# Kernel tuning notes

Measured on AMD Instinct MI355X. Metric: run time of the kernel, lower is better.

## Reference

```python
import jax, jax.numpy as jnp
import numpy as np

N_USER = 50000
N_ITEM = 100000
D = 64            # embed_size; layer_size = [64, 64, 64]
NL = 3            # number of propagation layers
NNZ = 2400000     # nonzeros of sparse Laplacian L
B = 1024          # batch of (user, pos_item, neg_item)
N = N_USER + N_ITEM


def setup_inputs() -> dict:
    key = jax.random.key(0)
    ks = jax.random.split(key, 20)
    inp = {}
    # learned parameters
    inp["user_emb"] = jax.random.normal(ks[0], (N_USER, D), jnp.float32) * 0.1
    inp["item_emb"] = jax.random.normal(ks[1], (N_ITEM, D), jnp.float32) * 0.1
    inp["lin1_w"] = jax.random.normal(ks[2], (4, D // 2), jnp.float32) * 0.5
    inp["lin1_b"] = jnp.zeros((D // 2,), jnp.float32)
    inp["lin2_w"] = jax.random.normal(ks[3], (D // 2, D), jnp.float32) * 0.2
    inp["lin2_b"] = jnp.zeros((D,), jnp.float32)
    inp["w1"] = jax.random.normal(ks[4], (NL, D, D), jnp.float32) * (1.0 / np.sqrt(D))
    inp["b1"] = jnp.zeros((NL, D), jnp.float32)
    inp["w2"] = jax.random.normal(ks[5], (NL, D, D), jnp.float32) * (1.0 / np.sqrt(D))
    inp["b2"] = jnp.zeros((NL, D), jnp.float32)
    # sparse normalized Laplacian L in COO form (eye_mat handled as +E)
    inp["lap_row"] = jax.random.randint(ks[6], (NNZ,), 0, N, jnp.int32)
    inp["lap_col"] = jax.random.randint(ks[7], (NNZ,), 0, N, jnp.int32)
    inp["lap_val"] = jax.random.uniform(ks[8], (NNZ,), jnp.float32) * (1.0 / 16.0)
    # forward args
    inp["user_idx"] = jax.random.randint(ks[9], (B,), 0, N_USER, jnp.int32)
    inp["user_feat"] = jax.random.normal(ks[10], (B, 4), jnp.float32)
    inp["pos_idx"] = jax.random.randint(ks[11], (B,), 0, N_ITEM, jnp.int32)
    inp["neg_idx"] = jax.random.randint(ks[12], (B,), 0, N_ITEM, jnp.int32)
    inp["mlp_ratio"] = jnp.float32(0.5)
    return inp


def reference(user_emb, item_emb, user_feat, lin1_w, lin1_b, lin2_w, lin2_b,
              w1, b1, w2, b2, lap_val, mlp_ratio,
              lap_row, lap_col, user_idx, pos_idx, neg_idx):
    n_user = user_emb.shape[0]
    n_nodes = user_emb.shape[0] + item_emb.shape[0]

    # user MLP: two stacked Linears (no activation in between, per Sequential)
    user_mlp = (user_feat @ lin1_w + lin1_b) @ lin2_w + lin2_b  # [B, D]
    # in-place no_grad embedding blend (stop_gradient mirrors torch.no_grad on mlp path)
    upd = user_emb[user_idx] * (1.0 - mlp_ratio) + jax.lax.stop_gradient(user_mlp) * mlp_ratio
    ue = user_emb.at[user_idx].set(upd)

    E = jnp.concatenate([ue, item_emb], axis=0)  # [N, D]

    def spmm(X):
        # L @ X via gather-multiply-segment_sum over COO nonzeros
        return jax.ops.segment_sum(lap_val[:, None] * X[lap_col], lap_row,
                                   num_segments=n_nodes)

    all_E = [E]
    for k in range(w1.shape[0]):
        L_E = spmm(E)                 # L @ E
        L_I_E = L_E + E               # (L + I) @ E
        msg = (L_I_E @ w1[k] + b1[k]) + ((L_E * E) @ w2[k] + b2[k])
        E = jax.nn.leaky_relu(msg, negative_slope=0.2)
        # F.normalize(E, p=2, dim=1) with eps=1e-12
        norm = E / jnp.maximum(jnp.linalg.norm(E, axis=1, keepdims=True), 1e-12)
        all_E.append(norm)

    all_E = jnp.concatenate(all_E, axis=1)  # [N, D*(NL+1)]
    users = all_E[:n_user]
    items = all_E[n_user:]
    return (users[user_idx], items[pos_idx], items[neg_idx])
```

## Files before the change

### kernel.cpp

```cpp
#include <hip/hip_runtime.h>
#include <hip/hip_bf16.h>

#define N_USERC 50000
#define N_ITEMC 100000
#define NNODE   150000
#define DIM     64
#define NLAYERS 3
#define NNZC    2400000
#define BATCH   1024

#define RPB     128
#define NBUCK   1172
#define NCHUNK  512
#define CHUNK   4688
#define CAPB    3072

using short8 = __attribute__((ext_vector_type(8))) short;
using f32x4  = __attribute__((ext_vector_type(4))) float;

__device__ __forceinline__ float bf2f(ushort u) {
    return __uint_as_float(((unsigned)u) << 16);
}
__device__ __forceinline__ ushort f2bf(float f) {
    unsigned u = __float_as_uint(f);
    u += 0x7FFF + ((u >> 16) & 1);
    return (ushort)(u >> 16);
}

__device__ __forceinline__ int block_excl_scan(int v, int* lds) {
    int lane = threadIdx.x & 63;
    int wid  = threadIdx.x >> 6;
    int nw   = (blockDim.x + 63) >> 6;
    int inc = v;
#pragma unroll
    for (int o = 1; o < 64; o <<= 1) {
        int n = __shfl_up(inc, o, 64);
        if (lane >= o) inc += n;
    }
    if (lane == 63) lds[wid] = inc;
    __syncthreads();
    if (wid == 0) {
        int tv = (lane < nw) ? lds[lane] : 0;
#pragma unroll
        for (int o = 1; o < 16; o <<= 1) {
            int n = __shfl_up(tv, o, 64);
            if (lane >= o) tv += n;
        }
        if (lane < nw) lds[lane] = tv;
    }
    __syncthreads();
    int woff = (wid == 0) ? 0 : lds[wid - 1];
    return woff + (inc - v);
}

__global__ void k_copy_E(const float* __restrict__ ue, const float* __restrict__ ie,
                         ushort* __restrict__ Ebf) {
    int i = blockIdx.x * blockDim.x + threadIdx.x;
    const int userEnd = N_USERC * DIM / 4;
    const int total   = NNODE * DIM / 4;
    if (i < total) {
        float4 v;
        if (i < userEnd) v = ((const float4*)ue)[i];
        else             v = ((const float4*)ie)[i - userEnd];
        ushort4 b;
        b.x = f2bf(v.x); b.y = f2bf(v.y); b.z = f2bf(v.z); b.w = f2bf(v.w);
        ((ushort4*)Ebf)[i] = b;
    }
}

__global__ void k_winner(const int* __restrict__ user_idx, int* __restrict__ winner) {
    int b = blockIdx.x * blockDim.x + threadIdx.x;
    if (b < BATCH) atomicMax(&winner[user_idx[b]], b);
}

__global__ void k_mlp_update(const float* __restrict__ user_emb,
                             const float* __restrict__ user_feat,
                             const float* __restrict__ l1w, const float* __restrict__ l1b,
                             const float* __restrict__ l2w, const float* __restrict__ l2b,
                             const float* __restrict__ ratio_p,
                             const int* __restrict__ user_idx,
                             const int* __restrict__ winner,
                             ushort* __restrict__ Ebf) {
    int b = blockIdx.x;
    int d = threadIdx.x;
    int u = user_idx[b];
    if (winner[u] != b) return;
    float ratio = ratio_p[0];
    float uf0 = user_feat[b * 4 + 0], uf1 = user_feat[b * 4 + 1];
    float uf2 = user_feat[b * 4 + 2], uf3 = user_feat[b * 4 + 3];
    float acc = l2b[d];
#pragma unroll
    for (int j = 0; j < 32; ++j) {
        float h = l1b[j] + uf0 * l1w[0 * 32 + j] + uf1 * l1w[1 * 32 + j]
                         + uf2 * l1w[2 * 32 + j] + uf3 * l1w[3 * 32 + j];
        acc += h * l2w[j * DIM + d];
    }
    float v = user_emb[u * DIM + d] * (1.f - ratio) + acc * ratio;
    Ebf[u * DIM + d] = f2bf(v);
}

__global__ void k_prepW(const float* __restrict__ w1, const float* __restrict__ w2,
                        ushort* __restrict__ Wtg) {
    int i = blockIdx.x * blockDim.x + threadIdx.x;
    if (i >= NLAYERS * 64 * 128) return;
    int layer = i >> 13;
    int rem = i & 8191;
    int n = rem >> 7, kk = rem & 127;
    float v = (kk < 64) ? w1[layer * 4096 + kk * 64 + n]
                        : w2[layer * 4096 + (kk - 64) * 64 + n];
    Wtg[i] = f2bf(v);
}

__global__ __launch_bounds__(256) void k_chunksort(const int* __restrict__ rows,
                                                   const int* __restrict__ cols,
                                                   const float* __restrict__ vals,
                                                   unsigned long long* __restrict__ tmp,
                                                   ushort* __restrict__ scanus) {
    __shared__ int hist[NBUCK];
    __shared__ int sutil[16];
    __shared__ unsigned long long stag[CHUNK];

    const int c = blockIdx.x;
    const int s = c * CHUNK;
    const int e = (s + CHUNK < NNZC) ? s + CHUNK : NNZC;
    const int t = threadIdx.x;

    for (int i = t; i < NBUCK; i += 256) hist[i] = 0;
    __syncthreads();
    for (int i = s + t; i < e; i += 256) atomicAdd(&hist[rows[i] >> 7], 1);
    __syncthreads();

    int loc[5];
    int sum = 0;
#pragma unroll
    for (int k = 0; k < 5; ++k) {
        int idx = t * 5 + k;
        int v = (idx < NBUCK) ? hist[idx] : 0;
        loc[k] = sum;
        sum += v;
    }
    int excl = block_excl_scan(sum, sutil);
#pragma unroll
    for (int k = 0; k < 5; ++k) {
        int idx = t * 5 + k;
        if (idx < NBUCK) hist[idx] = excl + loc[k];
    }
    __syncthreads();

    for (int i = t; i < NBUCK; i += 256) scanus[(size_t)c * (NBUCK + 1) + i] = (ushort)hist[i];
    if (t == 0) scanus[(size_t)c * (NBUCK + 1) + NBUCK] = (ushort)(e - s);
    __syncthreads();

    for (int i = s + t; i < e; i += 256) {
        int r = rows[i];
        int b = r >> 7, ro = r & 127;
        unsigned hi = ((unsigned)ro << 18) | (unsigned)cols[i];
        unsigned long long pk = ((unsigned long long)hi << 32) | (unsigned)__float_as_uint(vals[i]);
        int pos = atomicAdd(&hist[b], 1);
        stag[pos] = pk;
    }
    __syncthreads();

    int n = e - s;
    for (int i = t; i < n; i += 256) tmp[s + i] = stag[i];
}

__global__ void k_buckcnt(const ushort* __restrict__ scanus, int* __restrict__ bcnt) {
    int b = blockIdx.x * blockDim.x + threadIdx.x;
    if (b >= NBUCK) return;
    int sum = 0;
    for (int c = 0; c < NCHUNK; ++c) {
        const ushort* row = scanus + (size_t)c * (NBUCK + 1);
        sum += (int)row[b + 1] - (int)row[b];
    }
    bcnt[b] = sum;
}

__global__ __launch_bounds__(256) void k_bscan(const int* __restrict__ bcnt,
                                               int* __restrict__ bstart,
                                               int* __restrict__ rowptr) {
    __shared__ int sutil[16];
    int t = threadIdx.x;
    int loc[5];
    int sum = 0;
#pragma unroll
    for (int k = 0; k < 5; ++k) {
        int idx = t * 5 + k;
        int v = (idx < NBUCK) ? bcnt[idx] : 0;
        loc[k] = sum;
        sum += v;
    }
    int excl = block_excl_scan(sum, sutil);
#pragma unroll
    for (int k = 0; k < 5; ++k) {
        int idx = t * 5 + k;
        if (idx < NBUCK) bstart[idx] = excl + loc[k];
    }
    if (t == 0) { bstart[NBUCK] = NNZC; rowptr[NNODE] = NNZC; }
}

__global__ __launch_bounds__(256) void k_compact(const ushort* __restrict__ scanus,
                                                 const int* __restrict__ bstart,
                                                 const unsigned long long* __restrict__ tmp,
                                                 unsigned long long* __restrict__ csr,
                                                 int* __restrict__ rowptr) {
    __shared__ int runstart[NCHUNK];
    __shared__ int pref[NCHUNK + 1];
    __shared__ int sutil[16];
    __shared__ int rcur[RPB];
    __shared__ unsigned long long stag[CAPB];
    const int b = blockIdx.x;
    const int t = threadIdx.x;

    for (int r = t; r < NCHUNK; r += 256) {
        const ushort* row = scanus + (size_t)r * (NBUCK + 1);
        int s0 = row[b], s1 = row[b + 1];
        runstart[r] = r * CHUNK + s0;
        pref[r] = s1 - s0;
    }
    if (t < RPB) rcur[t] = 0;
    __syncthreads();
    int v0 = pref[t * 2], v1 = pref[t * 2 + 1];
    int sum = v0 + v1;
    int excl = block_excl_scan(sum, sutil);
    pref[t * 2] = excl;
    pref[t * 2 + 1] = excl + v0;
    if (t == 255) pref[NCHUNK] = excl + sum;
    __syncthreads();

    const int total = pref[NCHUNK];
    const int obase = bstart[b];

    if (total <= CAPB) {
        for (int r = t; r < NCHUNK; r += 256) {
            int p0 = pref[r], p1 = pref[r + 1];
            int rs = runstart[r];
            for (int i = p0; i < p1; ++i) stag[i] = tmp[rs + (i - p0)];
        }
        __syncthreads();
        for (int i = t; i < total; i += 256)
            atomicAdd(&rcur[(int)(stag[i] >> 50) & 127], 1);
        __syncthreads();
        int rv = (t < RPB) ? rcur[t] : 0;
        int rex = block_excl_scan(rv, sutil);
        if (t < RPB) {
            rcur[t] = rex;
            int grow = b * RPB + t;
            if (grow < NNODE) rowptr[grow] = obase + rex;
        }
        __syncthreads();
        for (int i = t; i < total; i += 256) {
            unsigned long long pk = stag[i];
            int ro = (int)(pk >> 50) & 127;
            int pos = atomicAdd(&rcur[ro], 1);
            csr[obase + pos] = pk;
        }
        return;
    }

    for (int i = t; i < total; i += 256) {
        int lo = 0, hi = NCHUNK - 1;
        while (lo < hi) {
            int mid = (lo + hi + 1) >> 1;
            if (pref[mid] <= i) lo = mid; else hi = mid - 1;
        }
        unsigned long long pk = tmp[runstart[lo] + (i - pref[lo])];
        atomicAdd(&rcur[(int)(pk >> 50) & 127], 1);
    }
    __syncthreads();
    int rv = (t < RPB) ? rcur[t] : 0;
    int rex = block_excl_scan(rv, sutil);
    if (t < RPB) {
        rcur[t] = rex;
        int grow = b * RPB + t;
        if (grow < NNODE) rowptr[grow] = obase + rex;
    }
    __syncthreads();
    for (int i = t; i < total; i += 256) {
        int lo = 0, hi = NCHUNK - 1;
        while (lo < hi) {
            int mid = (lo + hi + 1) >> 1;
            if (pref[mid] <= i) lo = mid; else hi = mid - 1;
        }
        unsigned long long pk = tmp[runstart[lo] + (i - pref[lo])];
        int ro = (int)(pk >> 50) & 127;
        int pos = atomicAdd(&rcur[ro], 1);
        csr[obase + pos] = pk;
    }
}

__global__ __launch_bounds__(256) void k_spmm(const int* __restrict__ rowptr,
                                              const unsigned long long* __restrict__ csr,
                                              const ushort* __restrict__ Ebf,
                                              float* __restrict__ L) {
    int lane = threadIdx.x & 63;
    int row  = blockIdx.x * 4 + (threadIdx.x >> 6);
    row = __builtin_amdgcn_readfirstlane(row);
    if (row >= NNODE) return;
    int s = __builtin_amdgcn_readfirstlane(rowptr[row]);
    int e = __builtin_amdgcn_readfirstlane(rowptr[row + 1]);
    const ushort* Ep = Ebf + lane;
    float acc = 0.f;
    int j = s;
    for (; j + 16 <= e; j += 16) {
        unsigned long long pk[16];
        float ev[16];
#pragma unroll
        for (int k = 0; k < 16; ++k) pk[k] = csr[j + k];
#pragma unroll
        for (int k = 0; k < 16; ++k) {
            int col = (int)(pk[k] >> 32) & 0x3FFFF;
            ev[k] = bf2f(Ep[col * DIM]);
        }
#pragma unroll
        for (int k = 0; k < 16; ++k)
            acc += __uint_as_float((unsigned)pk[k]) * ev[k];
    }
    if (j < e) {
        int m = e - j;
        unsigned long long pk[16];
        float ev[16];
#pragma unroll
        for (int k = 0; k < 16; ++k) {
            int idx = j + (k < m ? k : m - 1);
            pk[k] = csr[idx];
        }
#pragma unroll
        for (int k = 0; k < 16; ++k) {
            int col = (int)(pk[k] >> 32) & 0x3FFFF;
            ev[k] = bf2f(Ep[col * DIM]);
        }
#pragma unroll
        for (int k = 0; k < 16; ++k) {
            unsigned v = (k < m) ? (unsigned)pk[k] : 0u;
            acc += __uint_as_float(v) * ev[k];
        }
    }
    L[row * DIM + lane] = acc;
}

__global__ __launch_bounds__(256) void k_transform(const float* __restrict__ L,
                                                   const ushort* __restrict__ Ebf_in,
                                                   const ushort* __restrict__ Wtg,
                                                   const float* __restrict__ b1k,
                                                   const float* __restrict__ b2k,
                                                   ushort* __restrict__ Ebf_out) {
    __shared__ ushort A_s[64 * 136];
    __shared__ ushort W_s[64 * 136];
    __shared__ float  bias_s[64];

    const int t = threadIdx.x;
    const int rowbase = blockIdx.x * 64;
    if (t < 64) bias_s[t] = b1k[t] + b2k[t];

#pragma unroll
    for (int it = 0; it < 4; ++it) {
        int task = t + 256 * it;
        int n = task >> 4, k = (task & 15) * 8;
        uint4 wv = *(const uint4*)&Wtg[n * 128 + k];
        *(uint4*)&W_s[n * 136 + k] = wv;
    }
#pragma unroll
    for (int it = 0; it < 4; ++it) {
        int task = t + 256 * it;
        int rl = task >> 4, col = (task & 15) * 4;
        int row = rowbase + rl;
        float4 l4 = make_float4(0.f, 0.f, 0.f, 0.f);
        float e0 = 0.f, e1 = 0.f, e2 = 0.f, e3 = 0.f;
        if (row < NNODE) {
            l4 = *(const float4*)&L[row * 64 + col];
            ushort4 ub = *(const ushort4*)&Ebf_in[row * 64 + col];
            e0 = bf2f(ub.x); e1 = bf2f(ub.y); e2 = bf2f(ub.z); e3 = bf2f(ub.w);
        }
        *(ushort4*)&A_s[rl * 136 + col] =
            make_ushort4(f2bf(l4.x + e0), f2bf(l4.y + e1), f2bf(l4.z + e2), f2bf(l4.w + e3));
        *(ushort4*)&A_s[rl * 136 + 64 + col] =
            make_ushort4(f2bf(l4.x * e0), f2bf(l4.y * e1), f2bf(l4.z * e2), f2bf(l4.w * e3));
    }
    __syncthreads();

    const int w = t >> 6, l = t & 63;
    const int m16 = l & 15;
    const int q   = l >> 4;
    const int lm  = w * 16 + m16;

    f32x4 z = {0.f, 0.f, 0.f, 0.f};
    f32x4 acc[4] = {z, z, z, z};
#pragma unroll
    for (int ks = 0; ks < 4; ++ks) {
        short8 af = *(const short8*)&A_s[lm * 136 + ks * 32 + q * 8];
#pragma unroll
        for (int nt = 0; nt < 4; ++nt) {
            short8 wf = *(const short8*)&W_s[(nt * 16 + m16) * 136 + ks * 32 + q * 8];
            acc[nt] = __builtin_amdgcn_mfma_f32_16x16x32_bf16(af, wf, acc[nt], 0, 0, 0);
        }
    }
    __syncthreads();

    float* Cs = (float*)A_s;
#pragma unroll
    for (int nt = 0; nt < 4; ++nt) {
        int col = nt * 16 + m16;
#pragma unroll
        for (int r = 0; r < 4; ++r) {
            int lrow = w * 16 + q * 4 + r;
            Cs[lrow * 68 + col] = acc[nt][r];
        }
    }
    __syncthreads();

#pragma unroll
    for (int it = 0; it < 2; ++it) {
        int task = t + 256 * it;
        int rl = task >> 3, col = (task & 7) * 8;
        int row = rowbase + rl;
        if (row < NNODE) {
            float4 v0 = *(const float4*)&Cs[rl * 68 + col];
            float4 v1 = *(const float4*)&Cs[rl * 68 + col + 4];
            float o[8] = {v0.x, v0.y, v0.z, v0.w, v1.x, v1.y, v1.z, v1.w};
            ushort ob[8];
#pragma unroll
            for (int j = 0; j < 8; ++j) {
                float v = o[j] + bias_s[col + j];
                v = v >= 0.f ? v : 0.2f * v;
                ob[j] = f2bf(v);
            }
            uint4 pb;
            pb.x = (unsigned)ob[0] | ((unsigned)ob[1] << 16);
            pb.y = (unsigned)ob[2] | ((unsigned)ob[3] << 16);
            pb.z = (unsigned)ob[4] | ((unsigned)ob[5] << 16);
            pb.w = (unsigned)ob[6] | ((unsigned)ob[7] << 16);
            *(uint4*)&Ebf_out[row * 64 + col] = pb;
        }
    }
}

__global__ __launch_bounds__(256) void k_gather(const ushort* __restrict__ Ebf,
                                                const int* __restrict__ user_idx,
                                                const int* __restrict__ pos_idx,
                                                const int* __restrict__ neg_idx,
                                                float* __restrict__ out,
                                                int seg, int normalize) {
    int wid  = threadIdx.x >> 6;
    int lane = threadIdx.x & 63;
    int o = blockIdx.x * 4 + wid;
    if (o >= 3 * BATCH) return;
    int g = o >> 10, b = o & 1023;
    int row;
    if (g == 0)      row = user_idx[b];
    else if (g == 1) row = N_USERC + pos_idx[b];
    else             row = N_USERC + neg_idx[b];
    float v = bf2f(Ebf[row * DIM + lane]);
    if (normalize) {
        float ss = v * v;
#pragma unroll
        for (int m = 32; m; m >>= 1) ss += __shfl_xor(ss, m, 64);
        float nrm = sqrtf(ss);
        nrm = fmaxf(nrm, 1e-12f);
        v = v / nrm;
    }
    out[(g * BATCH + b) * 256 + seg * 64 + lane] = v;
}

extern "C" void kernel_launch(void* const* d_in, const int* in_sizes, int n_in,
                              void* d_out, int out_size, void* d_ws, size_t ws_size,
                              hipStream_t stream) {
    const float* user_emb  = (const float*)d_in[0];
    const float* item_emb  = (const float*)d_in[1];
    const float* lin1_w    = (const float*)d_in[2];
    const float* lin1_b    = (const float*)d_in[3];
    const float* lin2_w    = (const float*)d_in[4];
    const float* lin2_b    = (const float*)d_in[5];
    const float* w1        = (const float*)d_in[6];
    const float* b1        = (const float*)d_in[7];
    const float* w2        = (const float*)d_in[8];
    const float* b2        = (const float*)d_in[9];
    const int*   lap_row   = (const int*)d_in[10];
    const int*   lap_col   = (const int*)d_in[11];
    const float* lap_val   = (const float*)d_in[12];
    const int*   user_idx  = (const int*)d_in[13];
    const float* user_feat = (const float*)d_in[14];
    const int*   pos_idx   = (const int*)d_in[15];
    const int*   neg_idx   = (const int*)d_in[16];
    const float* mlp_ratio = (const float*)d_in[17];
    float* out = (float*)d_out;

    size_t off = 0;
    auto carve = [&](size_t bytes) { size_t r = off; off = (off + bytes + 255) & ~(size_t)255; return r; };
    size_t oL      = carve((size_t)NNODE * DIM * 4);
    size_t oEbf    = carve((size_t)NNODE * DIM * 2);
    size_t oCsr    = carve((size_t)NNZC * 8);
    size_t oScan   = carve((size_t)NCHUNK * (NBUCK + 1) * 2);
    size_t oBcnt   = carve((size_t)NBUCK * 4);
    size_t oBstart = carve((size_t)(NBUCK + 1) * 4);
    size_t oRowptr = carve((size_t)(NNODE + 1) * 4);
    size_t oWinner = carve((size_t)N_USERC * 4);
    (void)ws_size;

    char* base = (char*)d_ws;
    float*              L      = (float*)(base + oL);
    unsigned long long* tmp    = (unsigned long long*)(base + oL);
    ushort*             Ebf    = (ushort*)(base + oEbf);
    unsigned long long* csr    = (unsigned long long*)(base + oCsr);
    ushort*             scanus = (ushort*)(base + oScan);
    int*                bcnt   = (int*)(base + oBcnt);
    int*                bstart = (int*)(base + oBstart);
    int*                rowptr = (int*)(base + oRowptr);
    int*                winner = (int*)(base + oWinner);
    ushort*             Wtg    = (ushort*)(base + oScan);

    k_chunksort<<<NCHUNK, 256, 0, stream>>>(lap_row, lap_col, lap_val, tmp, scanus);
    k_buckcnt<<<(NBUCK + 255) / 256, 256, 0, stream>>>(scanus, bcnt);
    k_bscan<<<1, 256, 0, stream>>>(bcnt, bstart, rowptr);
    k_compact<<<NBUCK, 256, 0, stream>>>(scanus, bstart, tmp, csr, rowptr);

    k_prepW<<<(NLAYERS * 64 * 128 + 255) / 256, 256, 0, stream>>>(w1, w2, Wtg);
    hipMemsetAsync(winner, 0xFF, (size_t)N_USERC * 4, stream);
    k_copy_E<<<(NNODE * DIM / 4 + 255) / 256, 256, 0, stream>>>(user_emb, item_emb, Ebf);
    k_winner<<<(BATCH + 255) / 256, 256, 0, stream>>>(user_idx, winner);
    k_mlp_update<<<BATCH, 64, 0, stream>>>(user_emb, user_feat, lin1_w, lin1_b,
                                           lin2_w, lin2_b, mlp_ratio, user_idx, winner, Ebf);
    k_gather<<<(3 * BATCH) / 4, 256, 0, stream>>>(Ebf, user_idx, pos_idx, neg_idx, out, 0, 0);

    for (int k = 0; k < NLAYERS; ++k) {
        k_spmm<<<(NNODE + 3) / 4, 256, 0, stream>>>(rowptr, csr, Ebf, L);
        k_transform<<<(NNODE + 63) / 64, 256, 0, stream>>>(
            L, Ebf, Wtg + (size_t)k * 64 * 128, b1 + (size_t)k * DIM,
            b2 + (size_t)k * DIM, Ebf);
        k_gather<<<(3 * BATCH) / 4, 256, 0, stream>>>(Ebf, user_idx, pos_idx, neg_idx,
                                                      out, k + 1, 1);
    }
}
```

Before: 464.9 us.

## Fuse (L+I)E and L*E prep into SpMM, persistent grid, parallel bucket count

SpMM now computes both transform inputs, L_E+E and L_E*E, and writes them as bf16 into a 128-wide buffer with nontemporal stores. The transform kernel then just copies that buffer into LDS instead of reading fp32 L plus E. The SpMM becomes a grid-stride persistent kernel with 8/4-wide tail steps instead of a padded 16-wide tail. Bucket counting is split across 8 chunk partitions and summed in the scan kernel, raising parallelism in preprocessing. The bf16 intermediate equals the old rounding in the transform, so accuracy is unchanged, but the SpMM does more per-row work and issues an extra E read.

```diff
diff --git a/kernel.cpp b/kernel.cpp
--- a/kernel.cpp
+++ b/kernel.cpp
@@ -14,9 +14,11 @@
 #define NCHUNK  512
 #define CHUNK   4688
 #define CAPB    3072
+#define NPARTB  8
 
 using short8 = __attribute__((ext_vector_type(8))) short;
 using f32x4  = __attribute__((ext_vector_type(4))) float;
+using uintx4 = __attribute__((ext_vector_type(4))) unsigned;
 
 __device__ __forceinline__ float bf2f(ushort u) {
     return __uint_as_float(((unsigned)u) << 16);
@@ -165,18 +167,21 @@
     for (int i = t; i < n; i += 256) tmp[s + i] = stag[i];
 }
 
-__global__ void k_buckcnt(const ushort* __restrict__ scanus, int* __restrict__ bcnt) {
-    int b = blockIdx.x * blockDim.x + threadIdx.x;
+__global__ __launch_bounds__(256) void k_buckcnt(const ushort* __restrict__ scanus,
+                                                 int* __restrict__ bcntp) {
+    int b = blockIdx.x * 256 + threadIdx.x;
+    int g = blockIdx.y;
     if (b >= NBUCK) return;
+    int c0 = g * (NCHUNK / NPARTB), c1 = c0 + NCHUNK / NPARTB;
     int sum = 0;
-    for (int c = 0; c < NCHUNK; ++c) {
+    for (int c = c0; c < c1; ++c) {
         const ushort* row = scanus + (size_t)c * (NBUCK + 1);
         sum += (int)row[b + 1] - (int)row[b];
     }
-    bcnt[b] = sum;
-}
-
-__global__ __launch_bounds__(256) void k_bscan(const int* __restrict__ bcnt,
+    bcntp[g * NBUCK + b] = sum;
+}
+
+__global__ __launch_bounds__(256) void k_bscan(const int* __restrict__ bcntp,
                                                int* __restrict__ bstart,
                                                int* __restrict__ rowptr) {
     __shared__ int sutil[16];
@@ -186,7 +191,11 @@
 #pragma unroll
     for (int k = 0; k < 5; ++k) {
         int idx = t * 5 + k;
-        int v = (idx < NBUCK) ? bcnt[idx] : 0;
+        int v = 0;
+        if (idx < NBUCK) {
+#pragma unroll
+            for (int g = 0; g < NPARTB; ++g) v += bcntp[g * NBUCK + idx];
+        }
         loc[k] = sum;
         sum += v;
     }
@@ -289,58 +298,65 @@
     }
 }
 
+template<int K>
+__device__ __forceinline__ float gacc_full(const unsigned long long* __restrict__ csr,
+                                           const ushort* __restrict__ Ep, int j) {
+    unsigned long long pk[K];
+    float ev[K];
+#pragma unroll
+    for (int k = 0; k < K; ++k) pk[k] = csr[j + k];
+#pragma unroll
+    for (int k = 0; k < K; ++k) {
+        int col = (int)(pk[k] >> 32) & 0x3FFFF;
+        ev[k] = bf2f(Ep[col * DIM]);
+    }
+    float a = 0.f;
+#pragma unroll
+    for (int k = 0; k < K; ++k)
+        a += __uint_as_float((unsigned)pk[k]) * ev[k];
+    return a;
+}
+
 __global__ __launch_bounds__(256) void k_spmm(const int* __restrict__ rowptr,
                                               const unsigned long long* __restrict__ csr,
                                               const ushort* __restrict__ Ebf,
-                                              float* __restrict__ L) {
-    int lane = threadIdx.x & 63;
-    int row  = blockIdx.x * 4 + (threadIdx.x >> 6);
-    row = __builtin_amdgcn_readfirstlane(row);
-    if (row >= NNODE) return;
-    int s = __builtin_amdgcn_readfirstlane(rowptr[row]);
-    int e = __builtin_amdgcn_readfirstlane(rowptr[row + 1]);
+                                              ushort* __restrict__ Abf) {
+    const int lane = threadIdx.x & 63;
+    const int nw = gridDim.x * 4;
     const ushort* Ep = Ebf + lane;
-    float acc = 0.f;
-    int j = s;
-    for (; j + 16 <= e; j += 16) {
-        unsigned long long pk[16];
-        float ev[16];
-#pragma unroll
-        for (int k = 0; k < 16; ++k) pk[k] = csr[j + k];
-#pragma unroll
-        for (int k = 0; k < 16; ++k) {
-            int col = (int)(pk[k] >> 32) & 0x3FFFF;
-            ev[k] = bf2f(Ep[col * DIM]);
-        }
-#pragma unroll
-        for (int k = 0; k < 16; ++k)
-            acc += __uint_as_float((unsigned)pk[k]) * ev[k];
-    }
-    if (j < e) {
-        int m = e - j;
-        unsigned long long pk[16];
-        float ev[16];
-#pragma unroll
-        for (int k = 0; k < 16; ++k) {
-            int idx = j + (k < m ? k : m - 1);
-            pk[k] = csr[idx];
-        }
-#pragma unroll
-        for (int k = 0; k < 16; ++k) {
-            int col = (int)(pk[k] >> 32) & 0x3FFFF;
-            ev[k] = bf2f(Ep[col * DIM]);
-        }
-#pragma unroll
-        for (int k = 0; k < 16; ++k) {
-            unsigned v = (k < m) ? (unsigned)pk[k] : 0u;
-            acc += __uint_as_float(v) * ev[k];
-        }
-    }
-    L[row * DIM + lane] = acc;
-}
-
-__global__ __launch_bounds__(256) void k_transform(const float* __restrict__ L,
-                                                   const ushort* __restrict__ Ebf_in,
+    for (int row0 = blockIdx.x * 4 + (threadIdx.x >> 6); row0 < NNODE; row0 += nw) {
+        int row = __builtin_amdgcn_readfirstlane(row0);
+        int s = __builtin_amdgcn_readfirstlane(rowptr[row]);
+        int e = __builtin_amdgcn_readfirstlane(rowptr[row + 1]);
+        float acc = 0.f;
+        int j = s;
+        for (; j + 16 <= e; j += 16) acc += gacc_full<16>(csr, Ep, j);
+        if (j + 8 <= e) { acc += gacc_full<8>(csr, Ep, j); j += 8; }
+        if (j + 4 <= e) { acc += gacc_full<4>(csr, Ep, j); j += 4; }
+        if (j < e) {
+            int m = e - j;
+            unsigned long long pk[4];
+            float ev[4];
+#pragma unroll
+            for (int k = 0; k < 4; ++k) pk[k] = csr[j + (k < m ? k : m - 1)];
+#pragma unroll
+            for (int k = 0; k < 4; ++k) {
+                int col = (int)(pk[k] >> 32) & 0x3FFFF;
+                ev[k] = bf2f(Ep[col * DIM]);
+            }
+#pragma unroll
+            for (int k = 0; k < 4; ++k) {
+                unsigned v = (k < m) ? (unsigned)pk[k] : 0u;
+                acc += __uint_as_float(v) * ev[k];
+            }
+        }
+        float eo = bf2f(Ebf[row * DIM + lane]);
+        __builtin_nontemporal_store(f2bf(acc + eo), &Abf[row * 128 + lane]);
+        __builtin_nontemporal_store(f2bf(acc * eo), &Abf[row * 128 + 64 + lane]);
+    }
+}
+
+__global__ __launch_bounds__(256) void k_transform(const ushort* __restrict__ Abf,
                                                    const ushort* __restrict__ Wtg,
                                                    const float* __restrict__ b1k,
                                                    const float* __restrict__ b2k,
@@ -363,19 +379,12 @@
 #pragma unroll
     for (int it = 0; it < 4; ++it) {
         int task = t + 256 * it;
-        int rl = task >> 4, col = (task & 15) * 4;
+        int rl = task >> 4, k8 = (task & 15) * 8;
         int row = rowbase + rl;
-        float4 l4 = make_float4(0.f, 0.f, 0.f, 0.f);
-        float e0 = 0.f, e1 = 0.f, e2 = 0.f, e3 = 0.f;
-        if (row < NNODE) {
-            l4 = *(const float4*)&L[row * 64 + col];
-            ushort4 ub = *(const ushort4*)&Ebf_in[row * 64 + col];
-            e0 = bf2f(ub.x); e1 = bf2f(ub.y); e2 = bf2f(ub.z); e3 = bf2f(ub.w);
-        }
-        *(ushort4*)&A_s[rl * 136 + col] =
-            make_ushort4(f2bf(l4.x + e0), f2bf(l4.y + e1), f2bf(l4.z + e2), f2bf(l4.w + e3));
-        *(ushort4*)&A_s[rl * 136 + 64 + col] =
-            make_ushort4(f2bf(l4.x * e0), f2bf(l4.y * e1), f2bf(l4.z * e2), f2bf(l4.w * e3));
+        uintx4 v = {0u, 0u, 0u, 0u};
+        if (row < NNODE)
+            v = __builtin_nontemporal_load((const uintx4*)&Abf[row * 128 + k8]);
+        *(uintx4*)&A_s[rl * 136 + k8] = v;
     }
     __syncthreads();
 
@@ -495,23 +504,24 @@
     size_t oBstart = carve((size_t)(NBUCK + 1) * 4);
     size_t oRowptr = carve((size_t)(NNODE + 1) * 4);
     size_t oWinner = carve((size_t)N_USERC * 4);
-    (void)ws_size;
+    size_t oBcntP  = carve((size_t)NPARTB * NBUCK * 4);
+    (void)ws_size; (void)oBcnt;
 
     char* base = (char*)d_ws;
-    float*              L      = (float*)(base + oL);
+    ushort*             Abf    = (ushort*)(base + oL);
     unsigned long long* tmp    = (unsigned long long*)(base + oL);
     ushort*             Ebf    = (ushort*)(base + oEbf);
     unsigned long long* csr    = (unsigned long long*)(base + oCsr);
     ushort*             scanus = (ushort*)(base + oScan);
-    int*                bcnt   = (int*)(base + oBcnt);
     int*                bstart = (int*)(base + oBstart);
     int*                rowptr = (int*)(base + oRowptr);
     int*                winner = (int*)(base + oWinner);
+    int*                bcntp  = (int*)(base + oBcntP);
     ushort*             Wtg    = (ushort*)(base + oScan);
 
     k_chunksort<<<NCHUNK, 256, 0, stream>>>(lap_row, lap_col, lap_val, tmp, scanus);
-    k_buckcnt<<<(NBUCK + 255) / 256, 256, 0, stream>>>(scanus, bcnt);
-    k_bscan<<<1, 256, 0, stream>>>(bcnt, bstart, rowptr);
+    k_buckcnt<<<dim3(5, NPARTB), 256, 0, stream>>>(scanus, bcntp);
+    k_bscan<<<1, 256, 0, stream>>>(bcntp, bstart, rowptr);
     k_compact<<<NBUCK, 256, 0, stream>>>(scanus, bstart, tmp, csr, rowptr);
 
     k_prepW<<<(NLAYERS * 64 * 128 + 255) / 256, 256, 0, stream>>>(w1, w2, Wtg);
@@ -523,9 +533,9 @@
     k_gather<<<(3 * BATCH) / 4, 256, 0, stream>>>(Ebf, user_idx, pos_idx, neg_idx, out, 0, 0);
 
     for (int k = 0; k < NLAYERS; ++k) {
-        k_spmm<<<(NNODE + 3) / 4, 256, 0, stream>>>(rowptr, csr, Ebf, L);
+        k_spmm<<<2048, 256, 0, stream>>>(rowptr, csr, Ebf, Abf);
         k_transform<<<(NNODE + 63) / 64, 256, 0, stream>>>(
-            L, Ebf, Wtg + (size_t)k * 64 * 128, b1 + (size_t)k * DIM,
+            Abf, Wtg + (size_t)k * 64 * 128, b1 + (size_t)k * DIM,
             b2 + (size_t)k * DIM, Ebf);
         k_gather<<<(3 * BATCH) / 4, 256, 0, stream>>>(Ebf, user_idx, pos_idx, neg_idx,
                                                       out, k + 1, 1);
```

Measured after the change: 489.6 us. 5.3% more time.
